# Optimization experiments

Hardware: AMD Instinct MI355X
Metric: run time of the kernel (lower is better)

## Reference

```python
import jax, jax.numpy as jnp
import numpy as np

N, E, G = 8000, 32000, 256   # nodes, edges, graphs
F, H = 680, 10               # in-features, GAT heads
HF = F * H                   # 6800


def setup_inputs() -> dict:
    key = jax.random.key(0)
    ks = jax.random.split(key, 12)
    s = lambda i, shape, sc: (jax.random.normal(ks[i], shape, jnp.float32) * sc)
    x = jax.random.normal(ks[0], (N, F), jnp.float32)
    edge_index = jax.random.randint(ks[1], (2, E), 0, N)
    batch = jnp.arange(N) // (N // G)   # contiguous, every graph non-empty
    return dict(
        x=x, edge_index=edge_index, batch=batch,
        W_gat=s(2, (F, HF), 0.05), a_src=s(3, (H, F), 0.05), a_dst=s(4, (H, F), 0.05),
        b_gat=jnp.zeros((HF,), jnp.float32),
        W_gcn=s(5, (HF, HF), 0.01), b_gcn=jnp.zeros((HF,), jnp.float32),
        W1=s(6, (2 * HF, 512), 0.02), b1=jnp.zeros((512,), jnp.float32),
        W2=s(7, (512, 128), 0.05), b2=jnp.zeros((128,), jnp.float32),
        W3=s(8, (128, 64), 0.05), b3=jnp.zeros((64,), jnp.float32),
    )


def _self_loops(edge_index):
    loop = jnp.arange(N)
    return (jnp.concatenate([edge_index[0], loop]),
            jnp.concatenate([edge_index[1], loop]))


def _gat(x, src, dst, W, a_s, a_d, b):
    xh = (x @ W).reshape(N, H, F)                          # [N,H,F]
    al_s = jnp.einsum('nhf,hf->nh', xh, a_s)               # src attention logits
    al_d = jnp.einsum('nhf,hf->nh', xh, a_d)
    e = jax.nn.leaky_relu(al_s[src] + al_d[dst], 0.2)      # [Etot,H]
    m = jax.ops.segment_max(e, dst, num_segments=N)        # segment softmax over dst
    ex = jnp.exp(e - m[dst])
    z = jax.ops.segment_sum(ex, dst, num_segments=N)
    alpha = ex / (z[dst] + 1e-16)
    out = jax.ops.segment_sum(alpha[:, :, None] * xh[src], dst, num_segments=N)
    return out.reshape(N, HF) + b                          # concat heads + bias


def _gcn(x, src, dst, W, b):
    deg = jax.ops.segment_sum(jnp.ones_like(dst, jnp.float32), dst, num_segments=N)
    dinv = jax.lax.rsqrt(deg)                              # deg>=1 due to self-loops
    norm = dinv[src] * dinv[dst]
    xw = x @ W
    return jax.ops.segment_sum(norm[:, None] * xw[src], dst, num_segments=N) + b


def reference(x, edge_index, batch, W_gat, a_src, a_dst, b_gat, W_gcn, b_gcn,
              W1, b1, W2, b2, W3, b3):
    src, dst = _self_loops(edge_index)
    h = jax.nn.relu(_gat(x, src, dst, W_gat, a_src, a_dst, b_gat))  # dropout = id (eval)
    h = jax.nn.relu(_gcn(h, src, dst, W_gcn, b_gcn))
    gmp = jax.ops.segment_max(h, batch, num_segments=G)
    cnt = jax.ops.segment_sum(jnp.ones((N,), jnp.float32), batch, num_segments=G)
    gap = jax.ops.segment_sum(h, batch, num_segments=G) / cnt[:, None]
    g = jnp.concatenate([gmp, gap], axis=1)                # [G, 2*HF]
    g = jax.nn.relu(g @ W1 + b1)
    g = g @ W2 + b2
    return g @ W3 + b3                                     # [G, 64]
```

## Files before the change

### kernel.cpp

```cpp
#include <hip/hip_runtime.h>
#include <cstdint>
#include <cstddef>

#define DEVFN static __device__ __forceinline__

typedef __attribute__((ext_vector_type(8))) short short8;
typedef __attribute__((ext_vector_type(4))) float f32x4;

constexpr int NN  = 8000;
constexpr int NE  = 32000;
constexpr int ET  = NE + NN;
constexpr int NG  = 256;
constexpr int F   = 680;
constexpr int NH  = 10;
constexpr int HF  = 6800;

constexpr int MP   = 8192;
constexpr int KP1  = 704;
constexpr int NP   = 6912;
constexpr int KP2  = 6848;
constexpr int KM1P = 13632;

DEVFN unsigned short f2bf(float f) {
  unsigned u = __float_as_uint(f);
  u += 0x7fffu + ((u >> 16) & 1u);
  return (unsigned short)(u >> 16);
}
DEVFN float bf2f(unsigned short b) { return __uint_as_float(((unsigned)b) << 16); }

DEVFN int perm64(int k, int r) {
  return (((k >> 3) ^ (r & 7)) << 3) | (k & 7);
}

DEVFN void gload16(const void* g, void* l) {
  __builtin_amdgcn_global_load_lds(
      (const __attribute__((address_space(1))) unsigned int*)g,
      (__attribute__((address_space(3))) unsigned int*)l, 16, 0, 0);
}

DEVFN f32x4 mfma16(short8 a, short8 b, f32x4 c) {
  asm("v_mfma_f32_16x16x32_bf16 %0, %1, %2, %0" : "+v"(c) : "v"(a), "v"(b));
  return c;
}

template<int OUT_MODE, bool BIAS, bool RELU, bool SWZ>
__global__ __launch_bounds__(512, 2) void gemm256(
    const unsigned short* __restrict__ A, const unsigned short* __restrict__ BT,
    void* __restrict__ C, const float* __restrict__ bias,
    int K, int cstride, int nvalid, int Mt, int KC) {
  __shared__ alignas(16) char Lds[98304];
  const int tid = threadIdx.x;
  const int wave = tid >> 6, lane = tid & 63;
  const int wm = wave >> 2, wn = wave & 3;
  const int g4 = lane >> 4, l15 = lane & 15, l7 = lane & 7;

  int bm, bn;
  if (SWZ) {
    const int xcd = blockIdx.x & 7;
    const int j = blockIdx.x >> 3;
    bm = j & 63;
    bn = (j >> 6) * 8 + xcd;
    const int Nt = (nvalid + 255) >> 8;
    if (bn >= Nt) return;
  } else {
    bm = blockIdx.x % Mt;
    bn = blockIdx.x / Mt;
  }

  const int NTt = K >> 6;
  const int kb = blockIdx.z * KC;
  const int NT = min(KC, NTt - kb);
  const unsigned short* Ag = A + (size_t)bm * 128 * K + (size_t)kb * 64;
  const unsigned short* Bg = BT + (size_t)bn * 256 * K + (size_t)kb * 64;

  const size_t soff = (size_t)(tid >> 3) * K + (size_t)(tid & 7) * 8;

  auto stageA = [&](int t) {
    char* base = Lds + (t & 1) * 49152 + (wave << 10);
    const unsigned short* src = Ag + soff + (size_t)t * 64;
    gload16(src, base);
    gload16(src + (size_t)64 * K, base + 8192);
  };
  auto stageB = [&](int t) {
    char* base = Lds + (t & 1) * 49152 + 16384 + (wave << 10);
    const unsigned short* src = Bg + soff + (size_t)t * 64;
    gload16(src, base);
    gload16(src + (size_t)64 * K, base + 8192);
    gload16(src + (size_t)128 * K, base + 16384);
    gload16(src + (size_t)192 * K, base + 24576);
  };

  f32x4 acc[4][4];
#pragma unroll
  for (int i = 0; i < 4; i++)
#pragma unroll
    for (int j = 0; j < 4; j++) acc[i][j] = (f32x4){0.f, 0.f, 0.f, 0.f};

  short8 aR[2][2][2], bR[2][2][2];

#define RD_A(MH, AB) do {                                                        \
  _Pragma("unroll") for (int i2 = 0; i2 < 2; ++i2)                               \
  _Pragma("unroll") for (int ks = 0; ks < 2; ++ks)                               \
    aR[MH][i2][ks] = *(const short8*)((AB) + (wm * 64 + ((MH) * 2 + i2) * 16 + l15) * 128 \
                                      + ((((ks << 2) | g4) ^ l7) << 4));          \
} while (0)

#define RD_B(NH, BB) do {                                                        \
  _Pragma("unroll") for (int j2 = 0; j2 < 2; ++j2)                               \
  _Pragma("unroll") for (int ks = 0; ks < 2; ++ks)                               \
    bR[NH][j2][ks] = *(const short8*)((BB) + (wn * 64 + ((NH) * 2 + j2) * 16 + l15) * 128 \
                                      + ((((ks << 2) | g4) ^ l7) << 4));          \
} while (0)

#define MM(MH, NH) do {                                                          \
  __builtin_amdgcn_s_setprio(1);                                                 \
  _Pragma("unroll") for (int i2 = 0; i2 < 2; ++i2)                               \
  _Pragma("unroll") for (int j2 = 0; j2 < 2; ++j2)                               \
  _Pragma("unroll") for (int ks = 0; ks < 2; ++ks)                               \
    acc[(MH) * 2 + i2][(NH) * 2 + j2] =                                          \
        mfma16(aR[MH][i2][ks], bR[NH][j2][ks], acc[(MH) * 2 + i2][(NH) * 2 + j2]); \
  __builtin_amdgcn_s_setprio(0);                                                 \
} while (0)

  stageA(0); stageB(0);
  if (NT > 1) {
    stageA(1); stageB(1);
    asm volatile("s_waitcnt vmcnt(6)" ::: "memory");
  } else {
    asm volatile("s_waitcnt vmcnt(0)" ::: "memory");
  }
  asm volatile("s_barrier" ::: "memory");

  for (int t = 0; t < NT; ++t) {
    const char* Ab = Lds + (t & 1) * 49152;
    const char* Bb = Ab + 16384;
    const bool pf = (t + 2 < NT);

    RD_A(0, Ab);
    RD_B(0, Bb);
    RD_B(1, Bb);
    MM(0, 0);
    RD_A(1, Ab);
    MM(0, 1);
    asm volatile("s_barrier" ::: "memory");
    if (pf) stageB(t + 2);
    MM(1, 1);
    asm volatile("s_barrier" ::: "memory");
    if (pf) stageA(t + 2);
    MM(1, 0);
    if (pf) asm volatile("s_waitcnt vmcnt(6)" ::: "memory");
    else    asm volatile("s_waitcnt vmcnt(0)" ::: "memory");
    asm volatile("s_barrier" ::: "memory");
  }

#undef RD_A
#undef RD_B
#undef MM

  const int m0 = bm * 128 + wm * 64;
  const int n0 = bn * 256 + wn * 64;
  const int rb = g4 * 4;
#pragma unroll
  for (int i = 0; i < 4; i++) {
#pragma unroll
    for (int j = 0; j < 4; j++) {
      int c = n0 + j * 16 + l15;
      if (c >= nvalid) continue;
      float bv = BIAS ? bias[c] : 0.f;
#pragma unroll
      for (int tt = 0; tt < 4; tt++) {
        int r = m0 + i * 16 + rb + tt;
        float v = acc[i][j][tt] + bv;
        if (RELU) v = fmaxf(v, 0.f);
        if (OUT_MODE == 0) {
          ((float*)C)[(size_t)r * cstride + c] = v;
        } else if (OUT_MODE == 1) {
          ((unsigned short*)C)[(size_t)r * cstride + c] = f2bf(v);
        } else if (OUT_MODE == 2) {
          int pos = (c & ~63) + perm64(c & 63, r);
          ((unsigned short*)C)[(size_t)r * cstride + pos] = f2bf(v);
        } else {
          ((float*)C)[(size_t)blockIdx.z * (Mt * 128) * cstride + (size_t)r * cstride + c] = v;
        }
      }
    }
  }
}

template<bool RELU>
__global__ void finish_kernel(const float* __restrict__ acc, const float* __restrict__ bias,
                              unsigned short* __restrict__ out, int S, int M, int N) {
  int idx = blockIdx.x * 256 + threadIdx.x;
  if (idx >= M * N) return;
  int r = idx / N, c = idx - r * N;
  float s = bias[c];
  for (int k = 0; k < S; k++) s += acc[(size_t)k * M * N + (size_t)r * N + c];
  if (RELU) s = fmaxf(s, 0.f);
  out[(size_t)r * N + (c & ~63) + perm64(c & 63, r)] = f2bf(s);
}

__global__ void conv_x_kernel(const float* __restrict__ x, unsigned short* __restrict__ out) {
  int idx = blockIdx.x * 256 + threadIdx.x;
  constexpr int GR = KP1 / 4;
  if (idx >= MP * GR) return;
  int row = idx / GR, k = (idx - row * GR) * 4;
  unsigned short v[4] = {0, 0, 0, 0};
  if (row < NN && k < F) {
    const float* p = x + (size_t)row * F + k;
    v[0] = f2bf(p[0]); v[1] = f2bf(p[1]); v[2] = f2bf(p[2]); v[3] = f2bf(p[3]);
  }
  int pos = (k & ~63) + perm64(k & 63, row);
  uint2 pk;
  pk.x = (unsigned)v[0] | ((unsigned)v[1] << 16);
  pk.y = (unsigned)v[2] | ((unsigned)v[3] << 16);
  *(uint2*)&out[(size_t)row * KP1 + pos] = pk;
}

__global__ void convT_kernel(const float* __restrict__ in, unsigned short* __restrict__ out,
                             int K, int N, int KPad, int NPad) {
  __shared__ float tile[32][33];
  int n0 = blockIdx.x * 32, k0 = blockIdx.y * 32;
  int tx = threadIdx.x, ty = threadIdx.y;
#pragma unroll
  for (int i = 0; i < 4; i++) {
    int k = k0 + ty + i * 8, n = n0 + tx;
    tile[ty + i * 8][tx] = (k < K && n < N) ? in[(size_t)k * N + n] : 0.f;
  }
  __syncthreads();
#pragma unroll
  for (int i = 0; i < 4; i++) {
    int n = n0 + ty + i * 8, k = k0 + tx;
    if (n < NPad && k < KPad) {
      int pos = (k & ~63) + perm64(k & 63, n);
      out[(size_t)n * KPad + pos] = f2bf(tile[tx][ty + i * 8]);
    }
  }
}

__global__ void logits_kernel(const unsigned short* __restrict__ xh,
                              const float* __restrict__ a_src, const float* __restrict__ a_dst,
                              float* __restrict__ al_s, float* __restrict__ al_d) {
  int wid = blockIdx.x * 4 + (threadIdx.x >> 6);
  int lane = threadIdx.x & 63;
  int n = wid / NH, h = wid - n * NH;
  if (n >= NN) return;
  const unsigned short* row = xh + (size_t)n * NP + h * F;
  const float* as = a_src + h * F;
  const float* ad = a_dst + h * F;
  float ss = 0.f, sd = 0.f;
  for (int f0 = lane; f0 < F; f0 += 64) {
    float v = bf2f(row[f0]);
    ss += v * as[f0]; sd += v * ad[f0];
  }
#pragma unroll
  for (int o = 32; o > 0; o >>= 1) { ss += __shfl_down(ss, o); sd += __shfl_down(sd, o); }
  if (lane == 0) { al_s[wid] = ss; al_d[wid] = sd; }
}

__global__ void edge_count_kernel(const int* __restrict__ ei, int* __restrict__ deg) {
  int e = blockIdx.x * 256 + threadIdx.x;
  if (e >= ET) return;
  int d = (e < NE) ? ei[NE + e] : (e - NE);
  atomicAdd(&deg[d], 1);
}

__global__ void scan_kernel(const int* __restrict__ deg, int* __restrict__ rs,
                            int* __restrict__ cursor) {
  __shared__ int part[1024];
  int t = threadIdx.x;
  int base = t * 8, s = 0, loc[8];
#pragma unroll
  for (int i = 0; i < 8; i++) { loc[i] = s; int idx = base + i; s += (idx < NN) ? deg[idx] : 0; }
  part[t] = s;
  __syncthreads();
  for (int off = 1; off < 1024; off <<= 1) {
    int v = (t >= off) ? part[t - off] : 0;
    __syncthreads();
    part[t] += v;
    __syncthreads();
  }
  int pre = (t > 0) ? part[t - 1] : 0;
#pragma unroll
  for (int i = 0; i < 8; i++) {
    int idx = base + i;
    if (idx <= NN) { rs[idx] = pre + loc[i]; cursor[idx] = pre + loc[i]; }
  }
}

__global__ void edge_fill_kernel(const int* __restrict__ ei, int* __restrict__ cursor,
                                 int* __restrict__ eidx) {
  int e = blockIdx.x * 256 + threadIdx.x;
  if (e >= ET) return;
  int d = (e < NE) ? ei[NE + e] : (e - NE);
  int pos = atomicAdd(&cursor[d], 1);
  eidx[pos] = e;
}

__global__ void dinv_kernel(const int* __restrict__ deg, float* __restrict__ dinv) {
  int n = blockIdx.x * 256 + threadIdx.x;
  if (n < NN) dinv[n] = rsqrtf((float)max(deg[n], 1));
}

__global__ void alpha_kernel(const int* __restrict__ ei, const int* __restrict__ rs,
                             const int* __restrict__ eidx, const float* __restrict__ al_s,
                             const float* __restrict__ al_d, float* __restrict__ alpha) {
  int w = blockIdx.x * 256 + threadIdx.x;
  if (w >= NN * NH) return;
  int n = w / NH, h = w - n * NH;
  int s0 = rs[n], s1 = rs[n + 1];
  float ad = al_d[w];
  float m = -3.0e38f;
  for (int i = s0; i < s1; i++) {
    int e = eidx[i]; int s = (e < NE) ? ei[e] : (e - NE);
    float x = al_s[s * NH + h] + ad;
    x = (x > 0.f) ? x : 0.2f * x;
    m = fmaxf(m, x);
  }
  float z = 0.f;
  for (int i = s0; i < s1; i++) {
    int e = eidx[i]; int s = (e < NE) ? ei[e] : (e - NE);
    float x = al_s[s * NH + h] + ad;
    x = (x > 0.f) ? x : 0.2f * x;
    float ex = __expf(x - m);
    alpha[(size_t)i * NH + h] = ex;
    z += ex;
  }
  float inv = 1.f / (z + 1e-16f);
  for (int i = s0; i < s1; i++) alpha[(size_t)i * NH + h] *= inv;
}

DEVFN void axpy8(float al, uint4 r, float* a) {
  a[0] += al * bf2f((unsigned short)(r.x & 0xffff));
  a[1] += al * bf2f((unsigned short)(r.x >> 16));
  a[2] += al * bf2f((unsigned short)(r.y & 0xffff));
  a[3] += al * bf2f((unsigned short)(r.y >> 16));
  a[4] += al * bf2f((unsigned short)(r.z & 0xffff));
  a[5] += al * bf2f((unsigned short)(r.z >> 16));
  a[6] += al * bf2f((unsigned short)(r.w & 0xffff));
  a[7] += al * bf2f((unsigned short)(r.w >> 16));
}
DEVFN uint4 pack8(const float* a) {
  uint4 p;
  p.x = (unsigned)f2bf(a[0]) | ((unsigned)f2bf(a[1]) << 16);
  p.y = (unsigned)f2bf(a[2]) | ((unsigned)f2bf(a[3]) << 16);
  p.z = (unsigned)f2bf(a[4]) | ((unsigned)f2bf(a[5]) << 16);
  p.w = (unsigned)f2bf(a[6]) | ((unsigned)f2bf(a[7]) << 16);
  return p;
}

constexpr int MAXE = 256;

__global__ __launch_bounds__(256) void gat_agg_kernel(
    const unsigned short* __restrict__ xh, const int* __restrict__ ei,
    const int* __restrict__ rs, const int* __restrict__ eidx,
    const float* __restrict__ alpha, const float* __restrict__ bgat,
    unsigned short* __restrict__ hbf) {
  __shared__ int   Ls[MAXE];
  __shared__ float La[MAXE][NH];
  int n = blockIdx.x, t = threadIdx.x;
  int s0 = rs[n], d = rs[n + 1] - s0;
  int dc = min(d, MAXE);
  for (int i = t; i < dc; i += 256) {
    int e = eidx[s0 + i]; Ls[i] = (e < NE) ? ei[e] : (e - NE);
  }
  for (int j = t; j < dc * NH; j += 256)
    La[j / NH][j % NH] = alpha[(size_t)(s0 + j / NH) * NH + j % NH];
  __syncthreads();
  for (int c8 = t; c8 < KP2 / 8; c8 += 256) {
    int c = c8 * 8;
    int pos = (c & ~63) + ((((c >> 3) & 7) ^ (n & 7)) << 3);
    if (c >= HF) {
      *(uint4*)&hbf[(size_t)n * KP2 + pos] = make_uint4(0u, 0u, 0u, 0u);
      continue;
    }
    int h = c / F;
    float a[8] = {0.f, 0.f, 0.f, 0.f, 0.f, 0.f, 0.f, 0.f};
    for (int i = 0; i < dc; ++i)
      axpy8(La[i][h], *(const uint4*)&xh[(size_t)Ls[i] * NP + c], a);
    for (int i = MAXE; i < d; ++i) {
      int e = eidx[s0 + i]; int s = (e < NE) ? ei[e] : (e - NE);
      axpy8(alpha[(size_t)(s0 + i) * NH + h], *(const uint4*)&xh[(size_t)s * NP + c], a);
    }
#pragma unroll
    for (int q = 0; q < 8; ++q) a[q] = fmaxf(a[q] + bgat[c + q], 0.f);
    *(uint4*)&hbf[(size_t)n * KP2 + pos] = pack8(a);
  }
}

__global__ __launch_bounds__(256) void gcn_agg_kernel(
    const unsigned short* __restrict__ xw, const int* __restrict__ ei,
    const int* __restrict__ rs, const int* __restrict__ eidx,
    const float* __restrict__ dinv, const float* __restrict__ bgcn,
    unsigned short* __restrict__ h2) {
  __shared__ int   Ls[MAXE];
  __shared__ float Lw[MAXE];
  int n = blockIdx.x, t = threadIdx.x;
  int s0 = rs[n], d = rs[n + 1] - s0;
  int dc = min(d, MAXE);
  float dn = dinv[n];
  for (int i = t; i < dc; i += 256) {
    int e = eidx[s0 + i]; int s = (e < NE) ? ei[e] : (e - NE);
    Ls[i] = s; Lw[i] = dinv[s] * dn;
  }
  __syncthreads();
  for (int c8 = t; c8 < HF / 8; c8 += 256) {
    int c = c8 * 8;
    float a[8] = {0.f, 0.f, 0.f, 0.f, 0.f, 0.f, 0.f, 0.f};
    for (int i = 0; i < dc; ++i)
      axpy8(Lw[i], *(const uint4*)&xw[(size_t)Ls[i] * NP + c], a);
    for (int i = MAXE; i < d; ++i) {
      int e = eidx[s0 + i]; int s = (e < NE) ? ei[e] : (e - NE);
      axpy8(dinv[s] * dn, *(const uint4*)&xw[(size_t)s * NP + c], a);
    }
#pragma unroll
    for (int q = 0; q < 8; ++q) a[q] = fmaxf(a[q] + bgcn[c + q], 0.f);
    *(uint4*)&h2[(size_t)n * KP2 + c] = pack8(a);
  }
}

__global__ void pool_init_kernel(int* gstart, int* gend, int* gcnt) {
  int g = threadIdx.x;
  gstart[g] = 0x7fffffff; gend[g] = 0; gcnt[g] = 0;
}
__global__ void pool_scan_kernel(const int* __restrict__ batch, int* gstart, int* gend, int* gcnt) {
  int n = blockIdx.x * 256 + threadIdx.x;
  if (n >= NN) return;
  int b = batch[n];
  if (b >= 0 && b < NG) {
    atomicMin(&gstart[b], n);
    atomicMax(&gend[b], n + 1);
    atomicAdd(&gcnt[b], 1);
  }
}
__global__ void pool_kernel(const unsigned short* __restrict__ h2,
                            const int* __restrict__ gstart, const int* __restrict__ gend,
                            const int* __restrict__ gcnt, unsigned short* __restrict__ gbf) {
  int g = blockIdx.x, t = threadIdx.x;
  int s = gstart[g], e = gend[g];
  float inv = 1.f / (float)max(gcnt[g], 1);
  for (int c8 = t; c8 < HF / 8; c8 += 256) {
    int c = c8 * 8;
    float mx[8], sm[8];
#pragma unroll
    for (int q = 0; q < 8; ++q) { mx[q] = -3.0e38f; sm[q] = 0.f; }
    for (int n = s; n < e; ++n) {
      uint4 r = *(const uint4*)&h2[(size_t)n * KP2 + c];
      float v[8];
      v[0] = bf2f((unsigned short)(r.x & 0xffff)); v[1] = bf2f((unsigned short)(r.x >> 16));
      v[2] = bf2f((unsigned short)(r.y & 0xffff)); v[3] = bf2f((unsigned short)(r.y >> 16));
      v[4] = bf2f((unsigned short)(r.z & 0xffff)); v[5] = bf2f((unsigned short)(r.z >> 16));
      v[6] = bf2f((unsigned short)(r.w & 0xffff)); v[7] = bf2f((unsigned short)(r.w >> 16));
#pragma unroll
      for (int q = 0; q < 8; ++q) { mx[q] = fmaxf(mx[q], v[q]); sm[q] += v[q]; }
    }
#pragma unroll
    for (int q = 0; q < 8; ++q) sm[q] *= inv;
    int c2 = HF + c;
    int pos1 = (c & ~63) + ((((c >> 3) & 7) ^ (g & 7)) << 3);
    int pos2 = (c2 & ~63) + ((((c2 >> 3) & 7) ^ (g & 7)) << 3);
    *(uint4*)&gbf[(size_t)g * KM1P + pos1] = pack8(mx);
    *(uint4*)&gbf[(size_t)g * KM1P + pos2] = pack8(sm);
  }
}

extern "C" void kernel_launch(void* const* d_in, const int* in_sizes, int n_in,
                              void* d_out, int out_size, void* d_ws, size_t ws_size,
                              hipStream_t stream) {
  (void)in_sizes; (void)n_in; (void)out_size; (void)ws_size;
  const float* x     = (const float*)d_in[0];
  const int*   ei    = (const int*)d_in[1];
  const int*   batch = (const int*)d_in[2];
  const float* W_gat = (const float*)d_in[3];
  const float* a_src = (const float*)d_in[4];
  const float* a_dst = (const float*)d_in[5];
  const float* b_gat = (const float*)d_in[6];
  const float* W_gcn = (const float*)d_in[7];
  const float* b_gcn = (const float*)d_in[8];
  const float* W1    = (const float*)d_in[9];
  const float* b1    = (const float*)d_in[10];
  const float* W2    = (const float*)d_in[11];
  const float* b2    = (const float*)d_in[12];
  const float* W3    = (const float*)d_in[13];
  const float* b3    = (const float*)d_in[14];
  float* out = (float*)d_out;

  char* ws = (char*)d_ws;
  size_t off = 0;
  auto alloc = [&](size_t bytes) -> void* {
    void* p = ws + off;
    off += (bytes + 255) & ~(size_t)255;
    return p;
  };
  unsigned short* bufA  = (unsigned short*)alloc((size_t)MP * NP * 2);
  unsigned short* bufB  = (unsigned short*)alloc((size_t)MP * KP2 * 2);
  unsigned short* wgcnT = (unsigned short*)alloc((size_t)NP * KP2 * 2);
  unsigned short* xbf   = (unsigned short*)alloc((size_t)MP * KP1 * 2);
  unsigned short* wgatT = (unsigned short*)alloc((size_t)NP * KP1 * 2);
  unsigned short* w1T   = (unsigned short*)alloc((size_t)512 * KM1P * 2);
  unsigned short* gbf   = (unsigned short*)alloc((size_t)NG * KM1P * 2);
  unsigned short* w2T   = (unsigned short*)alloc((size_t)256 * 512 * 2);
  unsigned short* w3T   = (unsigned short*)alloc((size_t)256 * 128 * 2);
  unsigned short* g1bf  = (unsigned short*)alloc((size_t)NG * 512 * 2);
  unsigned short* g2bf  = (unsigned short*)alloc((size_t)NG * 128 * 2);
  float* accf  = (float*)alloc((size_t)32 * 256 * 512 * 4);
  float* al_s  = (float*)alloc((size_t)NN * NH * 4);
  float* al_d  = (float*)alloc((size_t)NN * NH * 4);
  float* alpha = (float*)alloc((size_t)ET * NH * 4);
  float* dinv  = (float*)alloc((size_t)NN * 4);
  int* deg    = (int*)alloc((size_t)NN * 4);
  int* rs     = (int*)alloc((size_t)(NN + 1) * 4);
  int* cursor = (int*)alloc((size_t)(NN + 1) * 4);
  int* eidx   = (int*)alloc((size_t)ET * 4);
  int* gstart = (int*)alloc((size_t)NG * 4);
  int* gend   = (int*)alloc((size_t)NG * 4);
  int* gcnt   = (int*)alloc((size_t)NG * 4);

  constexpr int GRID_SWZ = 8 * 64 * 4;

  conv_x_kernel<<<(MP * (KP1 / 4)) / 256, 256, 0, stream>>>(x, xbf);
  convT_kernel<<<dim3(NP / 32, KP1 / 32), dim3(32, 8), 0, stream>>>(W_gat, wgatT, F, HF, KP1, NP);
  convT_kernel<<<dim3(NP / 32, KP2 / 32), dim3(32, 8), 0, stream>>>(W_gcn, wgcnT, HF, HF, KP2, NP);
  convT_kernel<<<dim3(512 / 32, KM1P / 32), dim3(32, 8), 0, stream>>>(W1, w1T, 2 * HF, 512, KM1P, 512);
  convT_kernel<<<dim3(256 / 32, 512 / 32), dim3(32, 8), 0, stream>>>(W2, w2T, 512, 128, 512, 256);
  convT_kernel<<<dim3(256 / 32, 128 / 32), dim3(32, 8), 0, stream>>>(W3, w3T, 128, 64, 128, 256);
  hipMemsetAsync(deg, 0, (size_t)NN * 4, stream);
  hipMemsetAsync((char*)bufB + (size_t)NN * KP2 * 2, 0, (size_t)(MP - NN) * KP2 * 2, stream);
  hipMemsetAsync(gbf, 0, (size_t)NG * KM1P * 2, stream);

  gemm256<1, false, false, true><<<dim3(GRID_SWZ, 1, 1), 512, 0, stream>>>(
      xbf, wgatT, bufA, nullptr, KP1, NP, NP, 64, KP1 / 64);

  logits_kernel<<<(NN * NH) / 4, 256, 0, stream>>>(bufA, a_src, a_dst, al_s, al_d);

  edge_count_kernel<<<(ET + 255) / 256, 256, 0, stream>>>(ei, deg);
  scan_kernel<<<1, 1024, 0, stream>>>(deg, rs, cursor);
  edge_fill_kernel<<<(ET + 255) / 256, 256, 0, stream>>>(ei, cursor, eidx);
  dinv_kernel<<<(NN + 255) / 256, 256, 0, stream>>>(deg, dinv);

  alpha_kernel<<<(NN * NH + 255) / 256, 256, 0, stream>>>(ei, rs, eidx, al_s, al_d, alpha);

  gat_agg_kernel<<<NN, 256, 0, stream>>>(bufA, ei, rs, eidx, alpha, b_gat, bufB);

  gemm256<1, false, false, true><<<dim3(GRID_SWZ, 1, 1), 512, 0, stream>>>(
      bufB, wgcnT, bufA, nullptr, KP2, NP, NP, 64, KP2 / 64);

  gcn_agg_kernel<<<NN, 256, 0, stream>>>(bufA, ei, rs, eidx, dinv, b_gcn, bufB);

  pool_init_kernel<<<1, 256, 0, stream>>>(gstart, gend, gcnt);
  pool_scan_kernel<<<(NN + 255) / 256, 256, 0, stream>>>(batch, gstart, gend, gcnt);
  pool_kernel<<<NG, 256, 0, stream>>>(bufB, gstart, gend, gcnt, gbf);

  gemm256<3, false, false, false><<<dim3(2 * 2, 1, 31), 512, 0, stream>>>(
      gbf, w1T, accf, nullptr, KM1P, 512, 512, 2, 7);
  finish_kernel<true><<<(256 * 512) / 256, 256, 0, stream>>>(accf, b1, g1bf, 31, 256, 512);

  gemm256<3, false, false, false><<<dim3(2, 1, 4), 512, 0, stream>>>(
      g1bf, w2T, accf, nullptr, 512, 128, 128, 2, 2);
  finish_kernel<false><<<(256 * 128) / 256, 256, 0, stream>>>(accf, b2, g2bf, 4, 256, 128);

  gemm256<0, true, false, false><<<dim3(2, 1, 1), 512, 0, stream>>>(
      g2bf, w3T, out, b3, 128, 64, 64, 2, 2);
}
```

Before: 1.491 ms.

## Enlarge GEMM M-tile to 256 and load B fragments directly from pre-swizzled global layout

The GEMM block tile grows from 128x256 to 256x256, so each wave computes 128x64. The B operand is no longer staged through LDS. Weights are repacked once by a new convB kernel into an MFMA-fragment order, so each lane reads its short8 fragments straight from global memory into registers, double-buffered across k-steps. This roughly halves LDS use and the barriers per k-step, and raises arithmetic intensity per A load. The cost is more accumulator registers and exposed global-load latency on B, with all grids adjusted for the new M tiling.

After: 1.450 ms (median of 5 runs). -2.8%, faster.

```diff
diff --git a/kernel.cpp b/kernel.cpp
--- a/kernel.cpp
+++ b/kernel.cpp
@@ -48,7 +48,7 @@
     const unsigned short* __restrict__ A, const unsigned short* __restrict__ BT,
     void* __restrict__ C, const float* __restrict__ bias,
     int K, int cstride, int nvalid, int Mt, int KC) {
-  __shared__ alignas(16) char Lds[98304];
+  __shared__ alignas(16) char Lds[65536];
   const int tid = threadIdx.x;
   const int wave = tid >> 6, lane = tid & 63;
   const int wm = wave >> 2, wn = wave & 3;
@@ -58,8 +58,8 @@
   if (SWZ) {
     const int xcd = blockIdx.x & 7;
     const int j = blockIdx.x >> 3;
-    bm = j & 63;
-    bn = (j >> 6) * 8 + xcd;
+    bm = j & 31;
+    bn = (j >> 5) * 8 + xcd;
     const int Nt = (nvalid + 255) >> 8;
     if (bn >= Nt) return;
   } else {
@@ -67,101 +67,92 @@
     bn = blockIdx.x / Mt;
   }
 
-  const int NTt = K >> 6;
+  const int NKT = K >> 6;
   const int kb = blockIdx.z * KC;
-  const int NT = min(KC, NTt - kb);
-  const unsigned short* Ag = A + (size_t)bm * 128 * K + (size_t)kb * 64;
-  const unsigned short* Bg = BT + (size_t)bn * 256 * K + (size_t)kb * 64;
+  const int NT = min(KC, NKT - kb);
+  const unsigned short* Ag = A + (size_t)bm * 256 * K + (size_t)kb * 64;
+  const unsigned short* Bg2 = BT + (((size_t)(bn * 4 + wn) * NKT + kb) << 12)
+                                 + (size_t)lane * 8;
 
   const size_t soff = (size_t)(tid >> 3) * K + (size_t)(tid & 7) * 8;
 
   auto stageA = [&](int t) {
-    char* base = Lds + (t & 1) * 49152 + (wave << 10);
+    char* base = Lds + (t & 1) * 32768 + (wave << 10);
     const unsigned short* src = Ag + soff + (size_t)t * 64;
-    gload16(src, base);
-    gload16(src + (size_t)64 * K, base + 8192);
-  };
-  auto stageB = [&](int t) {
-    char* base = Lds + (t & 1) * 49152 + 16384 + (wave << 10);
-    const unsigned short* src = Bg + soff + (size_t)t * 64;
     gload16(src, base);
     gload16(src + (size_t)64 * K, base + 8192);
     gload16(src + (size_t)128 * K, base + 16384);
     gload16(src + (size_t)192 * K, base + 24576);
   };
 
-  f32x4 acc[4][4];
-#pragma unroll
-  for (int i = 0; i < 4; i++)
+  f32x4 acc[8][4];
+#pragma unroll
+  for (int i = 0; i < 8; i++)
 #pragma unroll
     for (int j = 0; j < 4; j++) acc[i][j] = (f32x4){0.f, 0.f, 0.f, 0.f};
 
-  short8 aR[2][2][2], bR[2][2][2];
-
-#define RD_A(MH, AB) do {                                                        \
-  _Pragma("unroll") for (int i2 = 0; i2 < 2; ++i2)                               \
+  short8 aF[4][2], bA[4][2], bB[4][2];
+
+#define LOAD_B(DST, T) do {                                                      \
+  const unsigned short* bp = Bg2 + ((size_t)(T) << 12);                          \
+  _Pragma("unroll") for (int j = 0; j < 4; ++j)                                  \
   _Pragma("unroll") for (int ks = 0; ks < 2; ++ks)                               \
-    aR[MH][i2][ks] = *(const short8*)((AB) + (wm * 64 + ((MH) * 2 + i2) * 16 + l15) * 128 \
-                                      + ((((ks << 2) | g4) ^ l7) << 4));          \
+    DST[j][ks] = *(const short8*)(bp + ((ks * 4 + j) << 9));                     \
 } while (0)
 
-#define RD_B(NH, BB) do {                                                        \
-  _Pragma("unroll") for (int j2 = 0; j2 < 2; ++j2)                               \
+#define RD_A(AB, H) do {                                                         \
+  _Pragma("unroll") for (int i2 = 0; i2 < 4; ++i2)                               \
   _Pragma("unroll") for (int ks = 0; ks < 2; ++ks)                               \
-    bR[NH][j2][ks] = *(const short8*)((BB) + (wn * 64 + ((NH) * 2 + j2) * 16 + l15) * 128 \
-                                      + ((((ks << 2) | g4) ^ l7) << 4));          \
+    aF[i2][ks] = *(const short8*)((AB) + (wm * 128 + ((H) * 4 + i2) * 16 + l15) * 128 \
+                                  + ((((ks << 2) | g4) ^ l7) << 4));             \
 } while (0)
 
-#define MM(MH, NH) do {                                                          \
+#define MM(H, BC) do {                                                           \
   __builtin_amdgcn_s_setprio(1);                                                 \
-  _Pragma("unroll") for (int i2 = 0; i2 < 2; ++i2)                               \
-  _Pragma("unroll") for (int j2 = 0; j2 < 2; ++j2)                               \
+  _Pragma("unroll") for (int i2 = 0; i2 < 4; ++i2)                               \
+  _Pragma("unroll") for (int j = 0; j < 4; ++j)                                  \
   _Pragma("unroll") for (int ks = 0; ks < 2; ++ks)                               \
-    acc[(MH) * 2 + i2][(NH) * 2 + j2] =                                          \
-        mfma16(aR[MH][i2][ks], bR[NH][j2][ks], acc[(MH) * 2 + i2][(NH) * 2 + j2]); \
+    acc[(H) * 4 + i2][j] = mfma16(aF[i2][ks], BC[j][ks], acc[(H) * 4 + i2][j]);  \
   __builtin_amdgcn_s_setprio(0);                                                 \
 } while (0)
 
-  stageA(0); stageB(0);
-  if (NT > 1) {
-    stageA(1); stageB(1);
-    asm volatile("s_waitcnt vmcnt(6)" ::: "memory");
-  } else {
-    asm volatile("s_waitcnt vmcnt(0)" ::: "memory");
-  }
+#define ITER(T, BC, BN) do {                                                     \
+  const char* Ab = Lds + ((T) & 1) * 32768;                                      \
+  const bool pf = (T) + 1 < NT;                                                  \
+  RD_A(Ab, 0);                                                                   \
+  if (pf) { stageA((T) + 1); LOAD_B(BN, (T) + 1); }                              \
+  MM(0, BC);                                                                     \
+  RD_A(Ab, 1);                                                                   \
+  MM(1, BC);                                                                     \
+  if (pf) {                                                                      \
+    asm volatile("s_waitcnt lgkmcnt(0)" ::: "memory");   \
+    asm volatile("s_waitcnt vmcnt(8)" ::: "memory");      \
+    asm volatile("s_barrier" ::: "memory");                                      \
+  }                                                                              \
+} while (0)
+
+  stageA(0);
+  LOAD_B(bA, 0);
+  asm volatile("s_waitcnt vmcnt(8)" ::: "memory");
   asm volatile("s_barrier" ::: "memory");
 
-  for (int t = 0; t < NT; ++t) {
-    const char* Ab = Lds + (t & 1) * 49152;
-    const char* Bb = Ab + 16384;
-    const bool pf = (t + 2 < NT);
-
-    RD_A(0, Ab);
-    RD_B(0, Bb);
-    RD_B(1, Bb);
-    MM(0, 0);
-    RD_A(1, Ab);
-    MM(0, 1);
-    asm volatile("s_barrier" ::: "memory");
-    if (pf) stageB(t + 2);
-    MM(1, 1);
-    asm volatile("s_barrier" ::: "memory");
-    if (pf) stageA(t + 2);
-    MM(1, 0);
-    if (pf) asm volatile("s_waitcnt vmcnt(6)" ::: "memory");
-    else    asm volatile("s_waitcnt vmcnt(0)" ::: "memory");
-    asm volatile("s_barrier" ::: "memory");
-  }
-
+  int t = 0;
+  for (; t + 1 < NT; t += 2) {
+    ITER(t, bA, bB);
+    ITER(t + 1, bB, bA);
+  }
+  if (t < NT) ITER(t, bA, bB);
+
+#undef ITER
+#undef MM
 #undef RD_A
-#undef RD_B
-#undef MM
-
-  const int m0 = bm * 128 + wm * 64;
+#undef LOAD_B
+
+  const int m0 = bm * 256 + wm * 128;
   const int n0 = bn * 256 + wn * 64;
   const int rb = g4 * 4;
 #pragma unroll
-  for (int i = 0; i < 4; i++) {
+  for (int i = 0; i < 8; i++) {
 #pragma unroll
     for (int j = 0; j < 4; j++) {
       int c = n0 + j * 16 + l15;
@@ -180,7 +171,7 @@
           int pos = (c & ~63) + perm64(c & 63, r);
           ((unsigned short*)C)[(size_t)r * cstride + pos] = f2bf(v);
         } else {
-          ((float*)C)[(size_t)blockIdx.z * (Mt * 128) * cstride + (size_t)r * cstride + c] = v;
+          ((float*)C)[(size_t)blockIdx.z * (Mt * 256) * cstride + (size_t)r * cstride + c] = v;
         }
       }
     }
@@ -216,25 +207,35 @@
   *(uint2*)&out[(size_t)row * KP1 + pos] = pk;
 }
 
-__global__ void convT_kernel(const float* __restrict__ in, unsigned short* __restrict__ out,
-                             int K, int N, int KPad, int NPad) {
-  __shared__ float tile[32][33];
-  int n0 = blockIdx.x * 32, k0 = blockIdx.y * 32;
-  int tx = threadIdx.x, ty = threadIdx.y;
-#pragma unroll
-  for (int i = 0; i < 4; i++) {
-    int k = k0 + ty + i * 8, n = n0 + tx;
-    tile[ty + i * 8][tx] = (k < K && n < N) ? in[(size_t)k * N + n] : 0.f;
+__global__ __launch_bounds__(256) void convB_kernel(
+    const float* __restrict__ W, unsigned short* __restrict__ out,
+    int K, int N, int KPad, int NPad) {
+  __shared__ float tile[64][17];
+  int n0 = blockIdx.x * 16, k0 = blockIdx.y * 64;
+  int t = threadIdx.x;
+#pragma unroll
+  for (int p = 0; p < 4; p++) {
+    int kr = p * 16 + (t >> 4), nc = t & 15;
+    int k = k0 + kr, n = n0 + nc;
+    tile[kr][nc] = (k < K && n < N) ? W[(size_t)k * N + n] : 0.f;
   }
   __syncthreads();
-#pragma unroll
-  for (int i = 0; i < 4; i++) {
-    int n = n0 + ty + i * 8, k = k0 + tx;
-    if (n < NPad && k < KPad) {
-      int pos = (k & ~63) + perm64(k & 63, n);
-      out[(size_t)n * KPad + pos] = f2bf(tile[tx][ty + i * 8]);
-    }
-  }
+  int ks = t >> 7;
+  int lane = (t >> 1) & 63;
+  int jh = (t & 1) * 4;
+  int g4 = lane >> 4, l15 = lane & 15;
+  int kk = (ks * 4 + g4) * 8 + jh;
+  unsigned short v[4];
+#pragma unroll
+  for (int q = 0; q < 4; q++) v[q] = f2bf(tile[kk + q][l15]);
+  int g64 = n0 >> 6, j = (n0 >> 4) & 3, kt = k0 >> 6;
+  int NKT = KPad >> 6;
+  size_t base = ((((size_t)g64 * NKT + kt) << 3) + (ks * 4 + j)) * 512
+              + (size_t)lane * 8 + jh;
+  uint2 pk;
+  pk.x = (unsigned)v[0] | ((unsigned)v[1] << 16);
+  pk.y = (unsigned)v[2] | ((unsigned)v[3] << 16);
+  *(uint2*)&out[base] = pk;
 }
 
 __global__ void logits_kernel(const unsigned short* __restrict__ xh,
@@ -493,13 +494,13 @@
   };
   unsigned short* bufA  = (unsigned short*)alloc((size_t)MP * NP * 2);
   unsigned short* bufB  = (unsigned short*)alloc((size_t)MP * KP2 * 2);
-  unsigned short* wgcnT = (unsigned short*)alloc((size_t)NP * KP2 * 2);
+  unsigned short* wgcnB = (unsigned short*)alloc((size_t)NP * KP2 * 2);
   unsigned short* xbf   = (unsigned short*)alloc((size_t)MP * KP1 * 2);
-  unsigned short* wgatT = (unsigned short*)alloc((size_t)NP * KP1 * 2);
-  unsigned short* w1T   = (unsigned short*)alloc((size_t)512 * KM1P * 2);
+  unsigned short* wgatB = (unsigned short*)alloc((size_t)NP * KP1 * 2);
+  unsigned short* w1B   = (unsigned short*)alloc((size_t)512 * KM1P * 2);
   unsigned short* gbf   = (unsigned short*)alloc((size_t)NG * KM1P * 2);
-  unsigned short* w2T   = (unsigned short*)alloc((size_t)256 * 512 * 2);
-  unsigned short* w3T   = (unsigned short*)alloc((size_t)256 * 128 * 2);
+  unsigned short* w2B   = (unsigned short*)alloc((size_t)256 * 512 * 2);
+  unsigned short* w3B   = (unsigned short*)alloc((size_t)256 * 128 * 2);
   unsigned short* g1bf  = (unsigned short*)alloc((size_t)NG * 512 * 2);
   unsigned short* g2bf  = (unsigned short*)alloc((size_t)NG * 128 * 2);
   float* accf  = (float*)alloc((size_t)32 * 256 * 512 * 4);
@@ -515,20 +516,20 @@
   int* gend   = (int*)alloc((size_t)NG * 4);
   int* gcnt   = (int*)alloc((size_t)NG * 4);
 
-  constexpr int GRID_SWZ = 8 * 64 * 4;
+  constexpr int GRID_SWZ = 8 * 32 * 4;
 
   conv_x_kernel<<<(MP * (KP1 / 4)) / 256, 256, 0, stream>>>(x, xbf);
-  convT_kernel<<<dim3(NP / 32, KP1 / 32), dim3(32, 8), 0, stream>>>(W_gat, wgatT, F, HF, KP1, NP);
-  convT_kernel<<<dim3(NP / 32, KP2 / 32), dim3(32, 8), 0, stream>>>(W_gcn, wgcnT, HF, HF, KP2, NP);
-  convT_kernel<<<dim3(512 / 32, KM1P / 32), dim3(32, 8), 0, stream>>>(W1, w1T, 2 * HF, 512, KM1P, 512);
-  convT_kernel<<<dim3(256 / 32, 512 / 32), dim3(32, 8), 0, stream>>>(W2, w2T, 512, 128, 512, 256);
-  convT_kernel<<<dim3(256 / 32, 128 / 32), dim3(32, 8), 0, stream>>>(W3, w3T, 128, 64, 128, 256);
+  convB_kernel<<<dim3(NP / 16, KP1 / 64), 256, 0, stream>>>(W_gat, wgatB, F, HF, KP1, NP);
+  convB_kernel<<<dim3(NP / 16, KP2 / 64), 256, 0, stream>>>(W_gcn, wgcnB, HF, HF, KP2, NP);
+  convB_kernel<<<dim3(512 / 16, KM1P / 64), 256, 0, stream>>>(W1, w1B, 2 * HF, 512, KM1P, 512);
+  convB_kernel<<<dim3(256 / 16, 512 / 64), 256, 0, stream>>>(W2, w2B, 512, 128, 512, 256);
+  convB_kernel<<<dim3(256 / 16, 128 / 64), 256, 0, stream>>>(W3, w3B, 128, 64, 128, 256);
   hipMemsetAsync(deg, 0, (size_t)NN * 4, stream);
   hipMemsetAsync((char*)bufB + (size_t)NN * KP2 * 2, 0, (size_t)(MP - NN) * KP2 * 2, stream);
   hipMemsetAsync(gbf, 0, (size_t)NG * KM1P * 2, stream);
 
   gemm256<1, false, false, true><<<dim3(GRID_SWZ, 1, 1), 512, 0, stream>>>(
-      xbf, wgatT, bufA, nullptr, KP1, NP, NP, 64, KP1 / 64);
+      xbf, wgatB, bufA, nullptr, KP1, NP, NP, 32, KP1 / 64);
 
   logits_kernel<<<(NN * NH) / 4, 256, 0, stream>>>(bufA, a_src, a_dst, al_s, al_d);
 
@@ -542,7 +543,7 @@
   gat_agg_kernel<<<NN, 256, 0, stream>>>(bufA, ei, rs, eidx, alpha, b_gat, bufB);
 
   gemm256<1, false, false, true><<<dim3(GRID_SWZ, 1, 1), 512, 0, stream>>>(
-      bufB, wgcnT, bufA, nullptr, KP2, NP, NP, 64, KP2 / 64);
+      bufB, wgcnB, bufA, nullptr, KP2, NP, NP, 32, KP2 / 64);
 
   gcn_agg_kernel<<<NN, 256, 0, stream>>>(bufA, ei, rs, eidx, dinv, b_gcn, bufB);
 
@@ -550,14 +551,14 @@
   pool_scan_kernel<<<(NN + 255) / 256, 256, 0, stream>>>(batch, gstart, gend, gcnt);
   pool_kernel<<<NG, 256, 0, stream>>>(bufB, gstart, gend, gcnt, gbf);
 
-  gemm256<3, false, false, false><<<dim3(2 * 2, 1, 31), 512, 0, stream>>>(
-      gbf, w1T, accf, nullptr, KM1P, 512, 512, 2, 7);
+  gemm256<3, false, false, false><<<dim3(2, 1, 31), 512, 0, stream>>>(
+      gbf, w1B, accf, nullptr, KM1P, 512, 512, 1, 7);
   finish_kernel<true><<<(256 * 512) / 256, 256, 0, stream>>>(accf, b1, g1bf, 31, 256, 512);
 
-  gemm256<3, false, false, false><<<dim3(2, 1, 4), 512, 0, stream>>>(
-      g1bf, w2T, accf, nullptr, 512, 128, 128, 2, 2);
+  gemm256<3, false, false, false><<<dim3(1, 1, 4), 512, 0, stream>>>(
+      g1bf, w2B, accf, nullptr, 512, 128, 128, 1, 2);
   finish_kernel<false><<<(256 * 128) / 256, 256, 0, stream>>>(accf, b2, g2bf, 4, 256, 128);
 
-  gemm256<0, true, false, false><<<dim3(2, 1, 1), 512, 0, stream>>>(
-      g2bf, w3T, out, b3, 128, 64, 64, 2, 2);
-}
+  gemm256<0, true, false, false><<<dim3(1, 1, 1), 512, 0, stream>>>(
+      g2bf, w3B, out, b3, 128, 64, 64, 1, 2);
+}
```
